# Performance work log

Measured on AMD Instinct MI355X. Metric: run time of the kernel, lower is better.

The kernel has to match this reference:

```python
import jax, jax.numpy as jnp
import numpy as np

# geomloss SamplesLoss('sinkhorn', blur=0.5, scaling=0.9, reach=None) defaults: p=2, debias=True
P = 2
BLUR = 0.5
SCALING = 0.9


def _sqdist_half(a, b):
    # C(x,y) = |x-y|^2 / 2  (geomloss p=2 cost), shape [N, M]
    a2 = jnp.sum(a * a, axis=1)
    b2 = jnp.sum(b * b, axis=1)
    return 0.5 * (a2[:, None] + b2[None, :]) - a @ b.T


def _softmin(eps, C, h):
    # softmin_tensorized: -eps * logsumexp_j( h_j - C_ij / eps ),  h = log-weights + dual/eps
    return -eps * jax.nn.logsumexp(h[None, :] - C / eps, axis=1)


def _eps_schedule(x, y):
    # geomloss epsilon_schedule: anneal eps from diameter^p down to blur^p by scaling^p
    xn, yn = np.asarray(x), np.asarray(y)
    mins = np.minimum(xn.min(axis=0), yn.min(axis=0))
    maxs = np.maximum(xn.max(axis=0), yn.max(axis=0))
    diameter = float(np.linalg.norm(maxs - mins))
    eps_list = [diameter ** P]
    eps_list += [float(np.exp(e)) for e in
                 np.arange(P * np.log(diameter), P * np.log(BLUR), P * np.log(SCALING))]
    eps_list += [BLUR ** P]
    return eps_list


def _sinkhorn_divergence(x, y, eps_list):
    N, M = x.shape[0], y.shape[0]
    C_xy = _sqdist_half(x, y)
    C_yx = C_xy.T
    C_xx = _sqdist_half(x, x)
    C_yy = _sqdist_half(y, y)
    a_log = jnp.full((N,), -float(np.log(N)), dtype=x.dtype)  # uniform weights, log domain
    b_log = jnp.full((M,), -float(np.log(M)), dtype=x.dtype)

    sg = jax.lax.stop_gradient
    Cxy_d, Cyx_d = sg(C_xy), sg(C_yx)
    Cxx_d, Cyy_d = sg(C_xx), sg(C_yy)

    # init at largest eps (= diameter^p)
    eps0 = eps_list[0]
    f_ba = _softmin(eps0, Cxy_d, b_log)
    g_ab = _softmin(eps0, Cyx_d, a_log)
    f_aa = _softmin(eps0, Cxx_d, a_log)
    g_bb = _softmin(eps0, Cyy_d, b_log)

    # symmetric (averaged) Sinkhorn updates along the eps-scaling schedule (no grad, like geomloss)
    for eps in eps_list:
        ft_ba = _softmin(eps, Cxy_d, b_log + g_ab / eps)
        gt_ab = _softmin(eps, Cyx_d, a_log + f_ba / eps)
        ft_aa = _softmin(eps, Cxx_d, a_log + f_aa / eps)
        gt_bb = _softmin(eps, Cyy_d, b_log + g_bb / eps)
        f_ba, g_ab = 0.5 * (f_ba + ft_ba), 0.5 * (g_ab + gt_ab)
        f_aa, g_bb = 0.5 * (f_aa + ft_aa), 0.5 * (g_bb + gt_bb)

    # last extrapolation at eps = blur^p; gradient flows only through the cost matrices here
    eps = eps_list[-1]
    f_ba, g_ab = (_softmin(eps, C_xy, sg(b_log + g_ab / eps)),
                  _softmin(eps, C_yx, sg(a_log + f_ba / eps)))
    f_aa = _softmin(eps, C_xx, sg(a_log + f_aa / eps))
    g_bb = _softmin(eps, C_yy, sg(b_log + g_bb / eps))

    # debiased divergence: <alpha, f_ba - f_aa> + <beta, g_ab - g_bb> (uniform weights -> mean)
    return jnp.mean(f_ba - f_aa) + jnp.mean(g_ab - g_bb)


def setup_inputs() -> dict:
    key = jax.random.key(0)
    kx, ky = jax.random.split(key)
    x = jax.random.normal(kx, (4096, 32), dtype=jnp.float32)
    y = jax.random.normal(ky, (4096, 32), dtype=jnp.float32)
    return {"x": x, "y": y}


def reference(x, y):
    eps_list = _eps_schedule(x, y)  # data-dependent schedule computed eagerly (as geomloss does)
    return _sinkhorn_divergence(x, y, eps_list)
```

## Files before the change

### kernel.cpp

```cpp
#include <hip/hip_runtime.h>
#include <math.h>

#define NPTS 4096
#define DIM  32
#define MAXSLOTS 50
#define NTHREADS 256
#define ITHREADS 512
#define NELEM 131072

#define WS_N2X   0
#define WS_N2Y   4096
#define WS_PMIN  8192
#define WS_PMAX  10240
#define WS_EPS   12288
#define WS_MODE  12352
#define WS_DUAL  12416
#define DUALSZ   16384
#define WS_BF    45184

#define M_SKIP   0
#define M_INIT   1
#define M_AVG    2
#define M_ASSIGN 3

typedef short   short8 __attribute__((ext_vector_type(8)));
typedef _Float16 half8 __attribute__((ext_vector_type(8)));
typedef float   f32x4  __attribute__((ext_vector_type(4)));

__device__ __forceinline__ float exp2fast(float a){
#if __has_builtin(__builtin_amdgcn_exp2f)
    return __builtin_amdgcn_exp2f(a);
#else
    return exp2f(a);
#endif
}
__device__ __forceinline__ float log2fast(float a){
#if __has_builtin(__builtin_amdgcn_logf)
    return __builtin_amdgcn_logf(a);
#else
    return log2f(a);
#endif
}

__global__ void sink_norms(const float* __restrict__ x, const float* __restrict__ y,
                           float* __restrict__ ws)
{
    int row = blockIdx.x * blockDim.x + threadIdx.x;
    const float* src = (row < NPTS) ? (x + (size_t)row * DIM)
                                    : (y + (size_t)(row - NPTS) * DIM);
    const float4* s4 = (const float4*)src;
    float acc = 0.f;
#pragma unroll
    for (int q = 0; q < 8; q++) {
        float4 v = s4[q];
        acc += v.x*v.x + v.y*v.y + v.z*v.z + v.w*v.w;
    }
    ws[row] = 0.5f * acc;
}

__global__ void sink_prep(const float* __restrict__ x, const float* __restrict__ y,
                          unsigned short* __restrict__ bf)
{
    int tid = blockIdx.x * 256 + threadIdx.x;
    int e = tid * 8;
    const float* src = (e < NELEM) ? (x + e) : (y + (e - NELEM));
    float4 v0 = ((const float4*)src)[0];
    float4 v1 = ((const float4*)src)[1];
    float vs[8] = {v0.x, v0.y, v0.z, v0.w, v1.x, v1.y, v1.z, v1.w};
    short hv[8];
#pragma unroll
    for (int i = 0; i < 8; i++) {
        union { _Float16 f; short s; } u;
        u.f = (_Float16)vs[i];
        hv[i] = u.s;
    }
    short8 hvec = {hv[0],hv[1],hv[2],hv[3],hv[4],hv[5],hv[6],hv[7]};
    *(short8*)((short*)bf + e) = hvec;
}

__global__ void sink_minmax(const float* __restrict__ x, const float* __restrict__ y,
                            float* __restrict__ ws)
{
    __shared__ float2 mm[8][32];
    int t = threadIdx.x;
    int d = t & 31, rg = t >> 5;
    float mn = 3.4e38f, mx = -3.4e38f;
#pragma unroll
    for (int k = 0; k < 16; k++) {
        int row = blockIdx.x * 128 + k * 8 + rg;
        const float* src = (row < NPTS) ? (x + (size_t)row * DIM)
                                        : (y + (size_t)(row - NPTS) * DIM);
        float v = src[d];
        mn = fminf(mn, v); mx = fmaxf(mx, v);
    }
    mm[rg][d] = make_float2(mn, mx);
    __syncthreads();
    if (t < 32) {
        float2 a = mm[0][t];
#pragma unroll
        for (int g = 1; g < 8; g++) {
            float2 b = mm[g][t];
            a.x = fminf(a.x, b.x); a.y = fmaxf(a.y, b.y);
        }
        ws[WS_PMIN + blockIdx.x * 32 + t] = a.x;
        ws[WS_PMAX + blockIdx.x * 32 + t] = a.y;
    }
}

__global__ void sink_sched(float* __restrict__ ws)
{
    __shared__ float mins[32], maxs[32];
    int t = threadIdx.x;
    if (t < 32) {
        float mn = 3.4e38f, mx = -3.4e38f;
        for (int b = 0; b < 64; b++) {
            mn = fminf(mn, ws[WS_PMIN + b * 32 + t]);
            mx = fmaxf(mx, ws[WS_PMAX + b * 32 + t]);
        }
        mins[t] = mn; maxs[t] = mx;
    }
    __syncthreads();
    if (t == 0) {
        float dia2 = 0.f;
        for (int d = 0; d < 32; d++) {
            float df = maxs[d] - mins[d];
            dia2 += df * df;
        }
        float dia = sqrtf(dia2);
        float* eps = ws + WS_EPS;
        int*  mode = (int*)(ws + WS_MODE);
        double ld    = log((double)dia);
        double start = 2.0 * ld;
        double stop  = 2.0 * log(0.5);
        double step  = 2.0 * log(0.9);
        int K = (int)ceil((stop - start) / step);
        if (K < 0) K = 0;
        if (K > MAXSLOTS - 5) K = MAXSLOTS - 5;
        eps[0] = dia * dia; mode[0] = M_INIT;
        eps[1] = dia * dia; mode[1] = M_AVG;
        for (int k = 0; k < K; k++) {
            eps[2 + k] = (float)exp(start + step * (double)k);
            mode[2 + k] = M_AVG;
        }
        eps[2 + K] = 0.25f; mode[2 + K] = M_AVG;
        eps[3 + K] = 0.25f; mode[3 + K] = M_ASSIGN;
        for (int s = 4 + K; s < MAXSLOTS; s++) { eps[s] = 0.25f; mode[s] = M_SKIP; }
    }
}

#define GLSE(T, R) \
    { float v0 = fmaf(ca##T[0][R], ie2, hpr[0]); \
      float v1 = fmaf(ca##T[1][R], ie2, hpr[1]); \
      float v2 = fmaf(ca##T[2][R], ie2, hpr[2]); \
      float v3 = fmaf(ca##T[3][R], ie2, hpr[3]); \
      float gm = fmaxf(fmaxf(v0, v1), v2); \
      float nm = fmaxf(fmaxf(gm, v3), ms##T[R]); \
      float er = exp2fast(ms##T[R] - nm); \
      float e0 = exp2fast(v0 - nm); \
      float e1 = exp2fast(v1 - nm); \
      float e2 = exp2fast(v2 - nm); \
      float e3 = exp2fast(v3 - nm); \
      ss##T[R] = fmaf(ss##T[R], er, (e0 + e1) + (e2 + e3)); \
      ms##T[R] = nm; }

__global__ __launch_bounds__(ITHREADS, 4) void sink_iter(float* __restrict__ ws, int slot)
{
    const int t = threadIdx.x;
    const int mode = ((const int*)(ws + WS_MODE))[slot];

    if (mode == M_SKIP) {
        int idx = blockIdx.x * ITHREADS + t;
        if (idx < DUALSZ)
            ws[WS_DUAL + ((slot + 1) & 1) * DUALSZ + idx] =
                ws[WS_DUAL + (slot & 1) * DUALSZ + idx];
        return;
    }

    const float eps     = ws[WS_EPS + slot];
    const float inv_eps = 1.0f / eps;
    const float L2E     = 1.4426950408889634f;
    const float LN2     = 0.6931471805599453f;
    const float ie2     = inv_eps * L2E;
    const float hbase   = -8.317766166719343f;
    const float don     = (mode == M_INIT) ? 0.0f : 1.0f;

    const int bm   = blockIdx.x >> 7;
    const int tile = blockIdx.x & 127;
    const int S    = (blockIdx.x * 5) & 31;
    const int rowIsX = (bm == 0 || bm == 2);
    const int colIsX = (bm == 1 || bm == 2);

    const short* bf = (const short*)(ws + WS_BF);
    const short* rbase = bf + (rowIsX ? 0 : NELEM);
    const short* cbase = bf + (colIsX ? 0 : NELEM);
    const float* rn2 = ws + (rowIsX ? WS_N2X : WS_N2Y);
    const float* cn2 = ws + (colIsX ? WS_N2X : WS_N2Y);

    const float* bufold = ws + WS_DUAL + (slot & 1) * DUALSZ;
    float*       bufnew = ws + WS_DUAL + ((slot + 1) & 1) * DUALSZ;
    const int dualsel = (bm == 0) ? 1 : (bm == 1) ? 0 : bm;
    const float* dual   = bufold + dualsel * NPTS;
    const float* oldout = bufold + bm * NPTS;
    float*       out    = bufnew + bm * NPTS;

    __shared__ float  hps[NPTS];
    __shared__ float2 parts[8][32];

    const int lane = t & 63;
    const int wv   = t >> 6;
    const int lr   = lane & 15;
    const int lk   = (lane >> 4) * 8;

    const int ar0 = tile * 32 + lr;
    const half8 a0 = *(const half8*)(rbase + ar0 * DIM + lk);
    const half8 a1 = *(const half8*)(rbase + (ar0 + 16) * DIM + lk);

#pragma unroll
    for (int q = 0; q < 8; q++) {
        int j = t + q * ITHREADS;
        hps[j] = (hbase + fmaf(don, dual[j], -cn2[j]) * inv_eps) * L2E;
    }
    __syncthreads();

    const int colbase = wv * 512;
    const short* cwb = cbase + (size_t)colbase * DIM;
    const int laneoff = lr * DIM + lk;
    const float* hpw = hps + colbase + lr;

    half8 bh[6];
    float hpv[6];
#pragma unroll
    for (int p = 0; p < 6; p++) {
        const int w = (p + S) & 31;
        bh[p]  = *(const half8*)(cwb + w * (16 * DIM) + laneoff);
        hpv[p] = hpw[w * 16];
    }

    float ms0[4] = {-INFINITY, -INFINITY, -INFINITY, -INFINITY};
    float ms1[4] = {-INFINITY, -INFINITY, -INFINITY, -INFINITY};
    float ss0[4] = {0.f, 0.f, 0.f, 0.f};
    float ss1[4] = {0.f, 0.f, 0.f, 0.f};

    f32x4 ca0[4], ca1[4];
    float hpr[4];

#pragma unroll
    for (int ct = 0; ct < 32; ct++) {
        const int sl = ct % 6;
        const half8 hB = bh[sl];
        hpr[ct & 3] = hpv[sl];
        f32x4 u0 = {0.f, 0.f, 0.f, 0.f};
        f32x4 u1 = {0.f, 0.f, 0.f, 0.f};
        u0 = __builtin_amdgcn_mfma_f32_16x16x32_f16(a0, hB, u0, 0, 0, 0);
        u1 = __builtin_amdgcn_mfma_f32_16x16x32_f16(a1, hB, u1, 0, 0, 0);
        if (ct < 26) {
            const int w = ((ct + 6) + S) & 31;
            bh[sl]  = *(const half8*)(cwb + w * (16 * DIM) + laneoff);
            hpv[sl] = hpw[w * 16];
        }
        ca0[ct & 3] = u0;
        ca1[ct & 3] = u1;
        if ((ct & 3) == 3) {
            GLSE(0, 0) GLSE(0, 1) GLSE(0, 2) GLSE(0, 3)
            GLSE(1, 0) GLSE(1, 1) GLSE(1, 2) GLSE(1, 3)
        }
    }

#pragma unroll
    for (int wm = 1; wm <= 8; wm <<= 1) {
#pragma unroll
        for (int r = 0; r < 4; r++) {
            float om, os, nm;
            om = __shfl_xor(ms0[r], wm, 64); os = __shfl_xor(ss0[r], wm, 64);
            nm = fmaxf(ms0[r], om);
            ss0[r] = fmaf(ss0[r], exp2fast(ms0[r] - nm), os * exp2fast(om - nm));
            ms0[r] = nm;
            om = __shfl_xor(ms1[r], wm, 64); os = __shfl_xor(ss1[r], wm, 64);
            nm = fmaxf(ms1[r], om);
            ss1[r] = fmaf(ss1[r], exp2fast(ms1[r] - nm), os * exp2fast(om - nm));
            ms1[r] = nm;
        }
    }
    if (lr == 0) {
        const int g4 = (lane >> 4) * 4;
#pragma unroll
        for (int r = 0; r < 4; r++) {
            parts[wv][g4 + r]      = make_float2(ms0[r], ss0[r]);
            parts[wv][16 + g4 + r] = make_float2(ms1[r], ss1[r]);
        }
    }
    __syncthreads();
    if (t < 32) {
        float2 p = parts[0][t];
        float m = p.x, s = p.y;
#pragma unroll
        for (int w2 = 1; w2 < 8; w2++) {
            float2 q = parts[w2][t];
            float nm = fmaxf(m, q.x);
            s = fmaf(s, exp2fast(m - nm), q.y * exp2fast(q.x - nm));
            m = nm;
        }
        const float lse = LN2 * (m + log2fast(s));
        const int row = tile * 32 + t;
        const float ft = rn2[row] - eps * lse;
        out[row] = (mode == M_AVG) ? 0.5f * (oldout[row] + ft) : ft;
    }
}

__global__ void sink_reduce(const float* __restrict__ ws, float* __restrict__ outp)
{
    __shared__ float red[NTHREADS];
    const float* b = ws + WS_DUAL;
    int t = threadIdx.x;
    float acc = 0.f;
    for (int i = t; i < NPTS; i += NTHREADS)
        acc += (b[i] - b[2 * NPTS + i]) + (b[NPTS + i] - b[3 * NPTS + i]);
    red[t] = acc;
    __syncthreads();
    for (int s = NTHREADS / 2; s > 0; s >>= 1) {
        if (t < s) red[t] += red[t + s];
        __syncthreads();
    }
    if (t == 0) outp[0] = red[0] * (1.0f / (float)NPTS);
}

extern "C" void kernel_launch(void* const* d_in, const int* in_sizes, int n_in,
                              void* d_out, int out_size, void* d_ws, size_t ws_size,
                              hipStream_t stream)
{
    const float* x = (const float*)d_in[0];
    const float* y = (const float*)d_in[1];
    float* ws  = (float*)d_ws;
    float* out = (float*)d_out;

    hipLaunchKernelGGL(sink_norms,  dim3(32),  dim3(NTHREADS), 0, stream, x, y, ws);
    hipLaunchKernelGGL(sink_prep,   dim3(128), dim3(NTHREADS), 0, stream, x, y,
                       (unsigned short*)(ws + WS_BF));
    hipLaunchKernelGGL(sink_minmax, dim3(64),  dim3(NTHREADS), 0, stream, x, y, ws);
    hipLaunchKernelGGL(sink_sched,  dim3(1),   dim3(NTHREADS), 0, stream, ws);
    for (int s = 0; s < MAXSLOTS; s++)
        hipLaunchKernelGGL(sink_iter, dim3(512), dim3(ITHREADS), 0, stream, ws, s);
    hipLaunchKernelGGL(sink_reduce, dim3(1), dim3(NTHREADS), 0, stream, ws, out);
}
```

Measured before the change: 887.8 us.

## Fuse setup kernels, drop LDS dual staging, skip copy in idle slots

Merges the norms, fp16 packing and min/max kernels into one setup launch. The iteration kernel no longer stages the log-weight vector in shared memory behind a barrier. Each lane instead computes its 32 needed entries straight into registers, and the B-tile prefetch depth drops from 6 to 4. Skipped slots now return immediately instead of copying the dual buffer, so the final reduce reads the parity recorded by the schedule kernel. This costs more registers per thread and one more usable schedule slot.

```diff
diff --git a/kernel.cpp b/kernel.cpp
--- a/kernel.cpp
+++ b/kernel.cpp
@@ -23,9 +23,9 @@
 #define M_AVG    2
 #define M_ASSIGN 3
 
-typedef short   short8 __attribute__((ext_vector_type(8)));
-typedef _Float16 half8 __attribute__((ext_vector_type(8)));
-typedef float   f32x4  __attribute__((ext_vector_type(4)));
+typedef short    short8 __attribute__((ext_vector_type(8)));
+typedef _Float16 half8  __attribute__((ext_vector_type(8)));
+typedef float    f32x4  __attribute__((ext_vector_type(4)));
 
 __device__ __forceinline__ float exp2fast(float a){
 #if __has_builtin(__builtin_amdgcn_exp2f)
@@ -42,28 +42,7 @@
 #endif
 }
 
-__global__ void sink_norms(const float* __restrict__ x, const float* __restrict__ y,
-                           float* __restrict__ ws)
-{
-    int row = blockIdx.x * blockDim.x + threadIdx.x;
-    const float* src = (row < NPTS) ? (x + (size_t)row * DIM)
-                                    : (y + (size_t)(row - NPTS) * DIM);
-    const float4* s4 = (const float4*)src;
-    float acc = 0.f;
-#pragma unroll
-    for (int q = 0; q < 8; q++) {
-        float4 v = s4[q];
-        acc += v.x*v.x + v.y*v.y + v.z*v.z + v.w*v.w;
-    }
-    ws[row] = 0.5f * acc;
-}
-
-__global__ void sink_prep(const float* __restrict__ x, const float* __restrict__ y,
-                          unsigned short* __restrict__ bf)
-{
-    int tid = blockIdx.x * 256 + threadIdx.x;
-    int e = tid * 8;
-    const float* src = (e < NELEM) ? (x + e) : (y + (e - NELEM));
+__device__ __forceinline__ short8 pack8(const float* src){
     float4 v0 = ((const float4*)src)[0];
     float4 v1 = ((const float4*)src)[1];
     float vs[8] = {v0.x, v0.y, v0.z, v0.w, v1.x, v1.y, v1.z, v1.w};
@@ -74,36 +53,58 @@
         u.f = (_Float16)vs[i];
         hv[i] = u.s;
     }
-    short8 hvec = {hv[0],hv[1],hv[2],hv[3],hv[4],hv[5],hv[6],hv[7]};
-    *(short8*)((short*)bf + e) = hvec;
-}
-
-__global__ void sink_minmax(const float* __restrict__ x, const float* __restrict__ y,
-                            float* __restrict__ ws)
+    short8 r = {hv[0],hv[1],hv[2],hv[3],hv[4],hv[5],hv[6],hv[7]};
+    return r;
+}
+
+__global__ void sink_setup(const float* __restrict__ x, const float* __restrict__ y,
+                           float* __restrict__ ws, unsigned short* __restrict__ bf)
 {
     __shared__ float2 mm[8][32];
-    int t = threadIdx.x;
-    int d = t & 31, rg = t >> 5;
-    float mn = 3.4e38f, mx = -3.4e38f;
-#pragma unroll
-    for (int k = 0; k < 16; k++) {
-        int row = blockIdx.x * 128 + k * 8 + rg;
-        const float* src = (row < NPTS) ? (x + (size_t)row * DIM)
-                                        : (y + (size_t)(row - NPTS) * DIM);
-        float v = src[d];
-        mn = fminf(mn, v); mx = fmaxf(mx, v);
-    }
-    mm[rg][d] = make_float2(mn, mx);
+    const int t = threadIdx.x;
+    const int b = blockIdx.x;
+    const int gtid = b * 256 + t;
+
+    {
+        int e = gtid * 8;
+        *(short8*)((short*)bf + e)         = pack8(x + e);
+        *(short8*)((short*)bf + NELEM + e) = pack8(y + e);
+    }
+    if (gtid < 2 * NPTS) {
+        const float* src = (gtid < NPTS) ? (x + (size_t)gtid * DIM)
+                                         : (y + (size_t)(gtid - NPTS) * DIM);
+        const float4* s4 = (const float4*)src;
+        float acc = 0.f;
+#pragma unroll
+        for (int q = 0; q < 8; q++) {
+            float4 v = s4[q];
+            acc += v.x*v.x + v.y*v.y + v.z*v.z + v.w*v.w;
+        }
+        ws[gtid] = 0.5f * acc;
+    }
+    {
+        int d = t & 31, rg = t >> 5;
+        float mn = 3.4e38f, mx = -3.4e38f;
+#pragma unroll
+        for (int k = 0; k < 16; k++) {
+            int row = b * 128 + k * 8 + rg;
+            const float* src = (row < NPTS) ? (x + (size_t)row * DIM)
+                                            : (y + (size_t)(row - NPTS) * DIM);
+            float v = src[d];
+            mn = fminf(mn, v); mx = fmaxf(mx, v);
+        }
+        mm[rg][d] = make_float2(mn, mx);
+    }
     __syncthreads();
     if (t < 32) {
         float2 a = mm[0][t];
 #pragma unroll
         for (int g = 1; g < 8; g++) {
-            float2 b = mm[g][t];
-            a.x = fminf(a.x, b.x); a.y = fmaxf(a.y, b.y);
-        }
-        ws[WS_PMIN + blockIdx.x * 32 + t] = a.x;
-        ws[WS_PMAX + blockIdx.x * 32 + t] = a.y;
+            float2 p = mm[g][t];
+            a.x = fminf(a.x, p.x); a.y = fmaxf(a.y, p.y);
+        }
+        ws[WS_PMIN + b * 32 + t] = a.x;
+        ws[WS_PMAX + b * 32 + t] = a.y;
     }
 }
 
@@ -135,7 +136,7 @@
         double step  = 2.0 * log(0.9);
         int K = (int)ceil((stop - start) / step);
         if (K < 0) K = 0;
-        if (K > MAXSLOTS - 5) K = MAXSLOTS - 5;
+        if (K > MAXSLOTS - 4) K = MAXSLOTS - 4;
         eps[0] = dia * dia; mode[0] = M_INIT;
         eps[1] = dia * dia; mode[1] = M_AVG;
         for (int k = 0; k < K; k++) {
@@ -145,14 +146,15 @@
         eps[2 + K] = 0.25f; mode[2 + K] = M_AVG;
         eps[3 + K] = 0.25f; mode[3 + K] = M_ASSIGN;
         for (int s = 4 + K; s < MAXSLOTS; s++) { eps[s] = 0.25f; mode[s] = M_SKIP; }
-    }
-}
-
-#define GLSE(T, R) \
-    { float v0 = fmaf(ca##T[0][R], ie2, hpr[0]); \
-      float v1 = fmaf(ca##T[1][R], ie2, hpr[1]); \
-      float v2 = fmaf(ca##T[2][R], ie2, hpr[2]); \
-      float v3 = fmaf(ca##T[3][R], ie2, hpr[3]); \
+        mode[62] = K + 4;
+    }
+}
+
+#define GLSE(T, R, G) \
+    { float v0 = fmaf(ca##T[0][R], ie2, hpq[(G)*4 + 0]); \
+      float v1 = fmaf(ca##T[1][R], ie2, hpq[(G)*4 + 1]); \
+      float v2 = fmaf(ca##T[2][R], ie2, hpq[(G)*4 + 2]); \
+      float v3 = fmaf(ca##T[3][R], ie2, hpq[(G)*4 + 3]); \
       float gm = fmaxf(fmaxf(v0, v1), v2); \
       float nm = fmaxf(fmaxf(gm, v3), ms##T[R]); \
       float er = exp2fast(ms##T[R] - nm); \
@@ -167,14 +169,7 @@
 {
     const int t = threadIdx.x;
     const int mode = ((const int*)(ws + WS_MODE))[slot];
-
-    if (mode == M_SKIP) {
-        int idx = blockIdx.x * ITHREADS + t;
-        if (idx < DUALSZ)
-            ws[WS_DUAL + ((slot + 1) & 1) * DUALSZ + idx] =
-                ws[WS_DUAL + (slot & 1) * DUALSZ + idx];
-        return;
-    }
+    if (mode == M_SKIP) return;
 
     const float eps     = ws[WS_EPS + slot];
     const float inv_eps = 1.0f / eps;
@@ -203,7 +198,6 @@
     const float* oldout = bufold + bm * NPTS;
     float*       out    = bufnew + bm * NPTS;
 
-    __shared__ float  hps[NPTS];
     __shared__ float2 parts[8][32];
 
     const int lane = t & 63;
@@ -215,55 +209,49 @@
     const half8 a0 = *(const half8*)(rbase + ar0 * DIM + lk);
     const half8 a1 = *(const half8*)(rbase + (ar0 + 16) * DIM + lk);
 
-#pragma unroll
-    for (int q = 0; q < 8; q++) {
-        int j = t + q * ITHREADS;
-        hps[j] = (hbase + fmaf(don, dual[j], -cn2[j]) * inv_eps) * L2E;
-    }
-    __syncthreads();
-
     const int colbase = wv * 512;
     const short* cwb = cbase + (size_t)colbase * DIM;
     const int laneoff = lr * DIM + lk;
-    const float* hpw = hps + colbase + lr;
-
-    half8 bh[6];
-    float hpv[6];
-#pragma unroll
-    for (int p = 0; p < 6; p++) {
+
+    float hpq[32];
+#pragma unroll
+    for (int p = 0; p < 32; p++) {
+        const int j = colbase + ((p + S) & 31) * 16 + lr;
+        hpq[p] = (hbase + fmaf(don, dual[j], -cn2[j]) * inv_eps) * L2E;
+    }
+
+    half8 bh[4];
+#pragma unroll
+    for (int p = 0; p < 4; p++) {
         const int w = (p + S) & 31;
-        bh[p]  = *(const half8*)(cwb + w * (16 * DIM) + laneoff);
-        hpv[p] = hpw[w * 16];
+        bh[p] = *(const half8*)(cwb + w * (16 * DIM) + laneoff);
     }
 
     float ms0[4] = {-INFINITY, -INFINITY, -INFINITY, -INFINITY};
     float ms1[4] = {-INFINITY, -INFINITY, -INFINITY, -INFINITY};
     float ss0[4] = {0.f, 0.f, 0.f, 0.f};
     float ss1[4] = {0.f, 0.f, 0.f, 0.f};
-
     f32x4 ca0[4], ca1[4];
-    float hpr[4];
-
-#pragma unroll
-    for (int ct = 0; ct < 32; ct++) {
-        const int sl = ct % 6;
-        const half8 hB = bh[sl];
-        hpr[ct & 3] = hpv[sl];
-        f32x4 u0 = {0.f, 0.f, 0.f, 0.f};
-        f32x4 u1 = {0.f, 0.f, 0.f, 0.f};
-        u0 = __builtin_amdgcn_mfma_f32_16x16x32_f16(a0, hB, u0, 0, 0, 0);
-        u1 = __builtin_amdgcn_mfma_f32_16x16x32_f16(a1, hB, u1, 0, 0, 0);
-        if (ct < 26) {
-            const int w = ((ct + 6) + S) & 31;
-            bh[sl]  = *(const half8*)(cwb + w * (16 * DIM) + laneoff);
-            hpv[sl] = hpw[w * 16];
-        }
-        ca0[ct & 3] = u0;
-        ca1[ct & 3] = u1;
-        if ((ct & 3) == 3) {
-            GLSE(0, 0) GLSE(0, 1) GLSE(0, 2) GLSE(0, 3)
-            GLSE(1, 0) GLSE(1, 1) GLSE(1, 2) GLSE(1, 3)
-        }
+
+#pragma unroll
+    for (int g = 0; g < 8; g++) {
+#pragma unroll
+        for (int sl = 0; sl < 4; sl++) {
+            const int ct = g * 4 + sl;
+            const half8 hB = bh[sl];
+            f32x4 u0 = {0.f, 0.f, 0.f, 0.f};
+            f32x4 u1 = {0.f, 0.f, 0.f, 0.f};
+            u0 = __builtin_amdgcn_mfma_f32_16x16x32_f16(a0, hB, u0, 0, 0, 0);
+            u1 = __builtin_amdgcn_mfma_f32_16x16x32_f16(a1, hB, u1, 0, 0, 0);
+            if (ct < 28) {
+                const int w = ((ct + 4) + S) & 31;
+                bh[sl] = *(const half8*)(cwb + w * (16 * DIM) + laneoff);
+            }
+            ca0[sl] = u0;
+            ca1[sl] = u1;
+        }
+        GLSE(0, 0, g) GLSE(0, 1, g) GLSE(0, 2, g) GLSE(0, 3, g)
+        GLSE(1, 0, g) GLSE(1, 1, g) GLSE(1, 2, g) GLSE(1, 3, g)
     }
 
 #pragma unroll
@@ -310,7 +298,8 @@
 __global__ void sink_reduce(const float* __restrict__ ws, float* __restrict__ outp)
 {
     __shared__ float red[NTHREADS];
-    const float* b = ws + WS_DUAL;
+    const int niter = ((const int*)(ws + WS_MODE))[62];
+    const float* b = ws + WS_DUAL + (niter & 1) * DUALSZ;
     int t = threadIdx.x;
     float acc = 0.f;
     for (int i = t; i < NPTS; i += NTHREADS)
@@ -333,11 +322,9 @@
     float* ws  = (float*)d_ws;
     float* out = (float*)d_out;
 
-    hipLaunchKernelGGL(sink_norms,  dim3(32),  dim3(NTHREADS), 0, stream, x, y, ws);
-    hipLaunchKernelGGL(sink_prep,   dim3(128), dim3(NTHREADS), 0, stream, x, y,
+    hipLaunchKernelGGL(sink_setup, dim3(64), dim3(NTHREADS), 0, stream, x, y, ws,
                        (unsigned short*)(ws + WS_BF));
-    hipLaunchKernelGGL(sink_minmax, dim3(64),  dim3(NTHREADS), 0, stream, x, y, ws);
-    hipLaunchKernelGGL(sink_sched,  dim3(1),   dim3(NTHREADS), 0, stream, ws);
+    hipLaunchKernelGGL(sink_sched, dim3(1),  dim3(NTHREADS), 0, stream, ws);
     for (int s = 0; s < MAXSLOTS; s++)
         hipLaunchKernelGGL(sink_iter, dim3(512), dim3(ITHREADS), 0, stream, ws, s);
     hipLaunchKernelGGL(sink_reduce, dim3(1), dim3(NTHREADS), 0, stream, ws, out);
```

Result: slower. 912.7 us (+2.8%).
